# Optimization experiments

Measured on AMD Instinct MI355X. Metric: run time of the kernel, lower is better.

## Reference

```python
import jax, jax.numpy as jnp
import numpy as np

EPS = 1e-5
SLOPE = 0.2  # LeakyReLU negative slope used by torch_points3d MLP

N = 16384
IN_MAIN, IN_MOD = 64, 128
NC_INNER, NC_QK, OUT_MAIN = 16, 8, 64


def setup_inputs() -> dict:
    key = jax.random.key(0)
    ks = jax.random.split(key, 8)
    def w(k, shape, fan_in):
        return jax.random.normal(k, shape, jnp.float32) * (1.0 / np.sqrt(fan_in))
    return dict(
        x_main=jax.random.normal(ks[0], (N, IN_MAIN), jnp.float32),
        x_mod=jax.random.normal(ks[1], (N, IN_MOD), jnp.float32),
        xyz=jax.random.uniform(ks[2], (N, 3), jnp.float32),
        W1=w(ks[3], (IN_MAIN + IN_MOD, NC_INNER), IN_MAIN + IN_MOD),
        g1=jnp.ones((NC_INNER,), jnp.float32),
        b1=jnp.zeros((NC_INNER,), jnp.float32),
        W2=w(ks[4], (NC_INNER, NC_INNER), NC_INNER),
        g2=jnp.ones((NC_INNER,), jnp.float32),
        b2=jnp.zeros((NC_INNER,), jnp.float32),
        Wq=w(ks[5], (NC_INNER, NC_QK), NC_INNER),
        Wk=w(ks[6], (NC_INNER, NC_QK), NC_INNER),
        Wv=w(ks[7], (NC_INNER, OUT_MAIN), NC_INNER),
    )


def _mlp_layer(x, W, g, b):
    # Linear(bias=False) -> BatchNorm1d (batch stats, training mode) -> LeakyReLU(0.2)
    h = x @ W
    m = jnp.mean(h, axis=0)
    v = jnp.var(h, axis=0)
    h = (h - m) * jax.lax.rsqrt(v + EPS) * g + b
    return jnp.where(h >= 0, h, SLOPE * h)


def reference(x_main, x_mod, xyz, W1, g1, b1, W2, g2, b2, Wq, Wk, Wv):
    # concat(3D feats, 2D feats) -> 2-layer MLP encoder E
    x = jnp.concatenate([x_main, x_mod], axis=-1)          # [N, in_main+in_mod]
    x = _mlp_layer(x, W1, g1, b1)                          # [N, nc_inner]
    x = _mlp_layer(x, W2, g2, b2)                          # [N, nc_inner]
    # global self-attention: full NxN scores (as in the original code)
    Q = x @ Wq                                             # [N, nc_qk]
    K = x @ Wk                                             # [N, nc_qk]
    V = x @ Wv                                             # [N, out_main]
    scale = 1.0 / jnp.sqrt(jnp.asarray(Q.shape[-1], Q.dtype))
    A = jax.nn.softmax((Q @ K.T) * scale, axis=1)          # [N, N]
    return A @ V                                           # [N, out_main]
```

## Files before the change

kernel.cpp:

```cpp
#include <hip/hip_runtime.h>
#include <stdint.h>

#define N_PTS 16384
#define EPSV 1e-5f
#define SLOPEV 0.2f

typedef __attribute__((ext_vector_type(8))) __bf16 bf16x8;
typedef __attribute__((ext_vector_type(4))) float f32x4;

union U4 { uint4 u; bf16x8 b; };

__device__ inline unsigned short f2bf(float x) {
    union { float f; uint32_t u; } v; v.f = x;
    uint32_t r = v.u + 0x7FFFu + ((v.u >> 16) & 1u);
    return (unsigned short)(r >> 16);
}
__device__ inline float bf2f(unsigned short b) {
    union { float f; uint32_t u; } v; v.u = ((uint32_t)b) << 16; return v.f;
}
__device__ inline unsigned cvt2(float lo, float hi) {
    union { __bf16 h[2]; unsigned u; } w;
    w.h[0] = (__bf16)lo; w.h[1] = (__bf16)hi;
    return w.u;
}

__global__ __launch_bounds__(128)
void enc1_kernel(const float* __restrict__ xm, const float* __restrict__ xd,
                 const float* __restrict__ W1, float* __restrict__ h1,
                 float* __restrict__ sum1, float* __restrict__ sumsq1) {
    __shared__ __align__(16) float Ws[192 * 16];
    __shared__ float ssum[16], ssq[16];
    const int tid = threadIdx.x;
    for (int i = tid; i < 192 * 16; i += 128) Ws[i] = W1[i];
    if (tid < 16) { ssum[tid] = 0.f; ssq[tid] = 0.f; }
    __syncthreads();
    const int row = blockIdx.x * 128 + tid;
    float h[16];
#pragma unroll
    for (int c = 0; c < 16; ++c) h[c] = 0.f;
    for (int j = 0; j < 64; j += 4) {
        const float4 x = *(const float4*)(xm + (size_t)row * 64 + j);
#pragma unroll
        for (int cc = 0; cc < 4; ++cc) {
            const f32x4 w0 = *(const f32x4*)&Ws[(j + 0) * 16 + cc * 4];
            const f32x4 w1 = *(const f32x4*)&Ws[(j + 1) * 16 + cc * 4];
            const f32x4 w2 = *(const f32x4*)&Ws[(j + 2) * 16 + cc * 4];
            const f32x4 w3 = *(const f32x4*)&Ws[(j + 3) * 16 + cc * 4];
#pragma unroll
            for (int e = 0; e < 4; ++e)
                h[cc * 4 + e] += x.x * w0[e] + x.y * w1[e] + x.z * w2[e] + x.w * w3[e];
        }
    }
    for (int j = 0; j < 128; j += 4) {
        const float4 x = *(const float4*)(xd + (size_t)row * 128 + j);
#pragma unroll
        for (int cc = 0; cc < 4; ++cc) {
            const f32x4 w0 = *(const f32x4*)&Ws[(64 + j + 0) * 16 + cc * 4];
            const f32x4 w1 = *(const f32x4*)&Ws[(64 + j + 1) * 16 + cc * 4];
            const f32x4 w2 = *(const f32x4*)&Ws[(64 + j + 2) * 16 + cc * 4];
            const f32x4 w3 = *(const f32x4*)&Ws[(64 + j + 3) * 16 + cc * 4];
#pragma unroll
            for (int e = 0; e < 4; ++e)
                h[cc * 4 + e] += x.x * w0[e] + x.y * w1[e] + x.z * w2[e] + x.w * w3[e];
        }
    }
#pragma unroll
    for (int c = 0; c < 16; c += 4)
        *(float4*)(h1 + (size_t)row * 16 + c) = make_float4(h[c], h[c + 1], h[c + 2], h[c + 3]);
#pragma unroll
    for (int c = 0; c < 16; ++c) {
        atomicAdd(&ssum[c], h[c]);
        atomicAdd(&ssq[c], h[c] * h[c]);
    }
    __syncthreads();
    if (tid < 16) { atomicAdd(&sum1[tid], ssum[tid]); atomicAdd(&sumsq1[tid], ssq[tid]); }
}

__global__ __launch_bounds__(64)
void finalize_bn(const float* __restrict__ sum, const float* __restrict__ sumsq,
                 const float* __restrict__ g, const float* __restrict__ b,
                 float* __restrict__ scale, float* __restrict__ shift) {
    const int c = threadIdx.x;
    if (c < 16) {
        const float mean = sum[c] * (1.f / N_PTS);
        const float var = sumsq[c] * (1.f / N_PTS) - mean * mean;
        const float sc = g[c] * rsqrtf(var + EPSV);
        scale[c] = sc;
        shift[c] = b[c] - mean * sc;
    }
}

__global__ __launch_bounds__(128)
void enc2_kernel(const float* __restrict__ h1, const float* __restrict__ scale1,
                 const float* __restrict__ shift1, const float* __restrict__ W2,
                 float* __restrict__ h2, float* __restrict__ sum2, float* __restrict__ sumsq2) {
    __shared__ __align__(16) float Ws[256];
    __shared__ float ssum[16], ssq[16];
    const int tid = threadIdx.x;
    for (int i = tid; i < 256; i += 128) Ws[i] = W2[i];
    if (tid < 16) { ssum[tid] = 0.f; ssq[tid] = 0.f; }
    __syncthreads();
    const int row = blockIdx.x * 128 + tid;
    float a[16];
#pragma unroll
    for (int j = 0; j < 16; j += 4) {
        const float4 hv = *(const float4*)(h1 + (size_t)row * 16 + j);
        a[j + 0] = hv.x * scale1[j + 0] + shift1[j + 0];
        a[j + 1] = hv.y * scale1[j + 1] + shift1[j + 1];
        a[j + 2] = hv.z * scale1[j + 2] + shift1[j + 2];
        a[j + 3] = hv.w * scale1[j + 3] + shift1[j + 3];
    }
#pragma unroll
    for (int j = 0; j < 16; ++j) a[j] = a[j] >= 0.f ? a[j] : SLOPEV * a[j];
    float h[16];
#pragma unroll
    for (int c = 0; c < 16; ++c) h[c] = 0.f;
#pragma unroll
    for (int j = 0; j < 16; ++j) {
#pragma unroll
        for (int cc = 0; cc < 4; ++cc) {
            const f32x4 wv = *(const f32x4*)&Ws[j * 16 + cc * 4];
#pragma unroll
            for (int e = 0; e < 4; ++e) h[cc * 4 + e] += a[j] * wv[e];
        }
    }
#pragma unroll
    for (int c = 0; c < 16; c += 4)
        *(float4*)(h2 + (size_t)row * 16 + c) = make_float4(h[c], h[c + 1], h[c + 2], h[c + 3]);
#pragma unroll
    for (int c = 0; c < 16; ++c) {
        atomicAdd(&ssum[c], h[c]);
        atomicAdd(&ssq[c], h[c] * h[c]);
    }
    __syncthreads();
    if (tid < 16) { atomicAdd(&sum2[tid], ssum[tid]); atomicAdd(&sumsq2[tid], ssq[tid]); }
}

__global__ __launch_bounds__(128)
void qkv_kernel(const float* __restrict__ h2, const float* __restrict__ scale2,
                const float* __restrict__ shift2, const float* __restrict__ Wq,
                const float* __restrict__ Wk, const float* __restrict__ Wv,
                unsigned short* __restrict__ Qp, unsigned short* __restrict__ Kp,
                unsigned short* __restrict__ Vt) {
    __shared__ __align__(16) float wqs[128], wks[128], wvs[1024];
    const int tid = threadIdx.x;
    for (int i = tid; i < 128; i += 128) { wqs[i] = Wq[i]; wks[i] = Wk[i]; }
    for (int i = tid; i < 1024; i += 128) wvs[i] = Wv[i];
    __syncthreads();
    const int row = blockIdx.x * 128 + tid;
    float a[16];
#pragma unroll
    for (int j = 0; j < 16; j += 4) {
        const float4 hv = *(const float4*)(h2 + (size_t)row * 16 + j);
        a[j + 0] = hv.x * scale2[j + 0] + shift2[j + 0];
        a[j + 1] = hv.y * scale2[j + 1] + shift2[j + 1];
        a[j + 2] = hv.z * scale2[j + 2] + shift2[j + 2];
        a[j + 3] = hv.w * scale2[j + 3] + shift2[j + 3];
    }
#pragma unroll
    for (int j = 0; j < 16; ++j) a[j] = a[j] >= 0.f ? a[j] : SLOPEV * a[j];

    const float SCL = (float)(1.4426950408889634 / 2.8284271247461903);
    union RowU { unsigned short s[32]; uint4 u[4]; } qr, kr;
#pragma unroll
    for (int o = 0; o < 8; ++o) {
        float sq = 0.f, sk = 0.f;
#pragma unroll
        for (int j = 0; j < 16; ++j) {
            sq += a[j] * wqs[j * 8 + o];
            sk += a[j] * wks[j * 8 + o];
        }
        const float qs = sq * SCL;
        const unsigned short qh = f2bf(qs);
        const unsigned short ql = f2bf(qs - bf2f(qh));
        qr.s[o] = qh; qr.s[8 + o] = ql; qr.s[16 + o] = qh; qr.s[24 + o] = 0;
        const unsigned short kh = f2bf(sk);
        const unsigned short kl = f2bf(sk - bf2f(kh));
        kr.s[o] = kh; kr.s[8 + o] = kh; kr.s[16 + o] = kl; kr.s[24 + o] = 0;
    }
#pragma unroll
    for (int k4 = 0; k4 < 4; ++k4) {
        *(uint4*)(Qp + (size_t)row * 32 + k4 * 8) = qr.u[k4];
        *(uint4*)(Kp + (size_t)row * 32 + k4 * 8) = kr.u[k4];
    }
#pragma unroll
    for (int d = 0; d < 64; ++d) {
        float sv = 0.f;
#pragma unroll
        for (int j = 0; j < 16; ++j) sv += a[j] * wvs[j * 64 + d];
        Vt[(size_t)d * N_PTS + row] = f2bf(sv);
    }
}

__global__ __launch_bounds__(512, 2)
void attn_kernel(const unsigned short* __restrict__ Qp,
                 const unsigned short* __restrict__ Kp,
                 const unsigned short* __restrict__ Vt,
                 float* __restrict__ partO, float* __restrict__ partML,
                 int kv_per_split) {
    __shared__ __align__(16) unsigned short vlds[64 * 136];
    const int tid = threadIdx.x;
    const int w = tid >> 6;
    const int l = tid & 63;
    const int g = l >> 4;
    const int c = l & 15;
    const int split = blockIdx.x;
    const int qbase = blockIdx.y * 512 + w * 64;
    const int kv0 = split * kv_per_split;
    const int nstage = kv_per_split >> 7;

    U4 qf[4];
#pragma unroll
    for (int qt = 0; qt < 4; ++qt)
        qf[qt].u = *(const uint4*)(Qp + (size_t)(qbase + qt * 16 + c) * 32 + g * 8);

    f32x4 acc[4][4];
#pragma unroll
    for (int qt = 0; qt < 4; ++qt)
#pragma unroll
        for (int dt = 0; dt < 4; ++dt) acc[qt][dt] = (f32x4){0.f, 0.f, 0.f, 0.f};
    float m_run[4], l_run[4];
#pragma unroll
    for (int qt = 0; qt < 4; ++qt) { m_run[qt] = -3.0e38f; l_run[qt] = 0.f; }

    for (int stage = 0; stage < nstage; ++stage) {
        const int kvs = kv0 + stage * 128;
        __syncthreads();
        for (int i = tid; i < 1024; i += 512) {
            const int r = i >> 4, ch = i & 15;
            *(uint4*)(vlds + r * 136 + ch * 8) =
                *(const uint4*)(Vt + (size_t)r * N_PTS + kvs + ch * 8);
        }
        __syncthreads();
        for (int sub = 0; sub < 4; ++sub) {
            const int kvg = kvs + sub * 32;
            U4 kf0, kf1;
            kf0.u = *(const uint4*)(Kp + (size_t)(kvg + c) * 32 + g * 8);
            kf1.u = *(const uint4*)(Kp + (size_t)(kvg + 16 + c) * 32 + g * 8);
            const f32x4 z4 = {0.f, 0.f, 0.f, 0.f};
            f32x4 s0[4], s1[4];
#pragma unroll
            for (int qt = 0; qt < 4; ++qt) {
                s0[qt] = __builtin_amdgcn_mfma_f32_16x16x32_bf16(kf0.b, qf[qt].b, z4, 0, 0, 0);
                s1[qt] = __builtin_amdgcn_mfma_f32_16x16x32_bf16(kf1.b, qf[qt].b, z4, 0, 0, 0);
            }
            float mloc[4];
            bool upd = false;
#pragma unroll
            for (int qt = 0; qt < 4; ++qt) {
                float mm = fmaxf(fmaxf(fmaxf(s0[qt][0], s0[qt][1]), fmaxf(s0[qt][2], s0[qt][3])),
                                 fmaxf(fmaxf(s1[qt][0], s1[qt][1]), fmaxf(s1[qt][2], s1[qt][3])));
                mm = fmaxf(mm, __shfl_xor(mm, 16));
                mm = fmaxf(mm, __shfl_xor(mm, 32));
                mloc[qt] = mm;
                upd = upd || (mm > m_run[qt]);
            }
            if (__any((int)upd)) {
#pragma unroll
                for (int qt = 0; qt < 4; ++qt) {
                    const float mn = fmaxf(m_run[qt], mloc[qt]);
                    const float al = __builtin_amdgcn_exp2f(m_run[qt] - mn);
                    l_run[qt] *= al;
#pragma unroll
                    for (int dt = 0; dt < 4; ++dt) acc[qt][dt] *= al;
                    m_run[qt] = mn;
                }
            }
            U4 pfb[4];
#pragma unroll
            for (int qt = 0; qt < 4; ++qt) {
                float p[8];
#pragma unroll
                for (int r = 0; r < 4; ++r) {
                    p[r] = __builtin_amdgcn_exp2f(s0[qt][r] - m_run[qt]);
                    p[4 + r] = __builtin_amdgcn_exp2f(s1[qt][r] - m_run[qt]);
                }
                float ps = ((p[0] + p[1]) + (p[2] + p[3])) + ((p[4] + p[5]) + (p[6] + p[7]));
                ps += __shfl_xor(ps, 16);
                ps += __shfl_xor(ps, 32);
                l_run[qt] += ps;
                const unsigned t0w0 = cvt2(p[0], p[1]);
                const unsigned t0w1 = cvt2(p[2], p[3]);
                const unsigned t1w0 = cvt2(p[4], p[5]);
                const unsigned t1w1 = cvt2(p[6], p[7]);
                const int srcA = ((g & 1) << 5) + c;
                const int srcB = srcA + 16;
                const unsigned a0 = __shfl(t0w0, srcA), a1 = __shfl(t0w1, srcA);
                const unsigned a2 = __shfl(t0w0, srcB), a3 = __shfl(t0w1, srcB);
                const unsigned b0 = __shfl(t1w0, srcA), b1 = __shfl(t1w1, srcA);
                const unsigned b2 = __shfl(t1w0, srcB), b3 = __shfl(t1w1, srcB);
                const bool lo2 = (g < 2);
                pfb[qt].u = make_uint4(lo2 ? a0 : b0, lo2 ? a1 : b1,
                                       lo2 ? a2 : b2, lo2 ? a3 : b3);
            }
#pragma unroll
            for (int dt = 0; dt < 4; ++dt) {
                U4 vf;
                vf.u = *(const uint4*)(vlds + (dt * 16 + c) * 136 + sub * 32 + g * 8);
#pragma unroll
                for (int qt = 0; qt < 4; ++qt)
                    acc[qt][dt] = __builtin_amdgcn_mfma_f32_16x16x32_bf16(vf.b, pfb[qt].b,
                                                                          acc[qt][dt], 0, 0, 0);
            }
        }
    }
#pragma unroll
    for (int qt = 0; qt < 4; ++qt) {
        const int q = qbase + qt * 16 + c;
#pragma unroll
        for (int dt = 0; dt < 4; ++dt)
            *(f32x4*)(partO + ((size_t)split * N_PTS + q) * 64 + dt * 16 + g * 4) = acc[qt][dt];
        if (g == 0) {
            partML[((size_t)split * N_PTS + q) * 2 + 0] = m_run[qt];
            partML[((size_t)split * N_PTS + q) * 2 + 1] = l_run[qt];
        }
    }
}

__global__ __launch_bounds__(256)
void merge_kernel(const float* __restrict__ partO, const float* __restrict__ partML,
                  float* __restrict__ out, int nsplit) {
    const int t = blockIdx.x * 256 + threadIdx.x;
    const int q = t >> 2, ch = t & 3;
    float M = -3.0e38f;
    for (int s = 0; s < nsplit; ++s)
        M = fmaxf(M, partML[((size_t)s * N_PTS + q) * 2 + 0]);
    float den = 0.f;
    f32x4 o0 = {0.f, 0.f, 0.f, 0.f}, o1 = o0, o2 = o0, o3 = o0;
    for (int s = 0; s < nsplit; ++s) {
        const float wgt = __builtin_amdgcn_exp2f(partML[((size_t)s * N_PTS + q) * 2 + 0] - M);
        den += wgt * partML[((size_t)s * N_PTS + q) * 2 + 1];
        const float* p = partO + ((size_t)s * N_PTS + q) * 64 + ch * 16;
        o0 += wgt * *(const f32x4*)(p + 0);
        o1 += wgt * *(const f32x4*)(p + 4);
        o2 += wgt * *(const f32x4*)(p + 8);
        o3 += wgt * *(const f32x4*)(p + 12);
    }
    const float inv = 1.f / den;
    float* po = out + (size_t)q * 64 + ch * 16;
    *(f32x4*)(po + 0) = o0 * inv;
    *(f32x4*)(po + 4) = o1 * inv;
    *(f32x4*)(po + 8) = o2 * inv;
    *(f32x4*)(po + 12) = o3 * inv;
}

extern "C" void kernel_launch(void* const* d_in, const int* in_sizes, int n_in,
                              void* d_out, int out_size, void* d_ws, size_t ws_size,
                              hipStream_t stream) {
    const float* xm = (const float*)d_in[0];
    const float* xd = (const float*)d_in[1];
    const float* W1 = (const float*)d_in[3];
    const float* g1 = (const float*)d_in[4];
    const float* b1 = (const float*)d_in[5];
    const float* W2 = (const float*)d_in[6];
    const float* g2 = (const float*)d_in[7];
    const float* b2 = (const float*)d_in[8];
    const float* Wq = (const float*)d_in[9];
    const float* Wk = (const float*)d_in[10];
    const float* Wv = (const float*)d_in[11];
    float* out = (float*)d_out;
    char* ws = (char*)d_ws;

    float* sum1 = (float*)(ws + 0);
    float* sumsq1 = (float*)(ws + 64);
    float* sum2 = (float*)(ws + 128);
    float* sumsq2 = (float*)(ws + 192);
    float* scale1 = (float*)(ws + 256);
    float* shift1 = (float*)(ws + 320);
    float* scale2 = (float*)(ws + 384);
    float* shift2 = (float*)(ws + 448);
    float* h1 = (float*)(ws + (1u << 20));
    float* h2 = (float*)(ws + (2u << 20));
    unsigned short* Qp = (unsigned short*)(ws + (3u << 20));
    unsigned short* Kp = (unsigned short*)(ws + (4u << 20));
    unsigned short* Vt = (unsigned short*)(ws + (5u << 20));
    float* partML = (float*)(ws + (7u << 20));
    float* partO = (float*)(ws + (8u << 20));

    int nsplit = 8;
    while (nsplit > 1 && (8u + 4u * (unsigned)nsplit) * (1u << 20) > ws_size) nsplit >>= 1;
    const int kv_per_split = N_PTS / nsplit;

    hipMemsetAsync(ws, 0, 256, stream);
    hipLaunchKernelGGL(enc1_kernel, dim3(128), dim3(128), 0, stream, xm, xd, W1, h1, sum1, sumsq1);
    hipLaunchKernelGGL(finalize_bn, dim3(1), dim3(64), 0, stream, sum1, sumsq1, g1, b1, scale1, shift1);
    hipLaunchKernelGGL(enc2_kernel, dim3(128), dim3(128), 0, stream, h1, scale1, shift1, W2, h2, sum2, sumsq2);
    hipLaunchKernelGGL(finalize_bn, dim3(1), dim3(64), 0, stream, sum2, sumsq2, g2, b2, scale2, shift2);
    hipLaunchKernelGGL(qkv_kernel, dim3(128), dim3(128), 0, stream, h2, scale2, shift2, Wq, Wk, Wv, Qp, Kp, Vt);
    hipLaunchKernelGGL(attn_kernel, dim3(nsplit, 32), dim3(512), 0, stream, Qp, Kp, Vt, partO, partML, kv_per_split);
    hipLaunchKernelGGL(merge_kernel, dim3(256), dim3(256), 0, stream, partO, partML, out, nsplit);
}
```

Baseline: 382.6 us.

## Switch attention to 32x32x16 MFMA with swizzled V LDS and lazy rescale

The attention kernel now uses 32x32x16 bf16 MFMA tiles with one 32-query tile per wave instead of four 16x16x32 tiles. It drops the cross-lane shuffles that repacked P, because the 32x32 output layout feeds the PV MFMA directly. The Q/K split-bf16 packing is reduced from three terms to two MFMA passes, and V in LDS uses an XOR swizzle instead of padding. The running max is only updated when it grows by more than 8 (log2 units), block occupancy is raised to 4 per CU and the grid doubles. Per-thread accumulator registers and max/shuffle work drop, but lazy rescaling risks larger exponent ranges and the bf16 P precision is unchanged.

Measured after the change: 327.0 us. 14.5% less time.

```diff
diff --git a/kernel.cpp b/kernel.cpp
--- a/kernel.cpp
+++ b/kernel.cpp
@@ -7,6 +7,7 @@
 
 typedef __attribute__((ext_vector_type(8))) __bf16 bf16x8;
 typedef __attribute__((ext_vector_type(4))) float f32x4;
+typedef __attribute__((ext_vector_type(16))) float f32x16;
 
 union U4 { uint4 u; bf16x8 b; };
 
@@ -161,7 +162,8 @@
     for (int j = 0; j < 16; ++j) a[j] = a[j] >= 0.f ? a[j] : SLOPEV * a[j];
 
     const float SCL = (float)(1.4426950408889634 / 2.8284271247461903);
-    union RowU { unsigned short s[32]; uint4 u[4]; } qr, kr;
+    union Row16 { unsigned short s[16]; uint4 u[2]; } qr;
+    union Row32 { unsigned short s[32]; uint4 u[4]; } kr;
 #pragma unroll
     for (int o = 0; o < 8; ++o) {
         float sq = 0.f, sk = 0.f;
@@ -173,16 +175,16 @@
         const float qs = sq * SCL;
         const unsigned short qh = f2bf(qs);
         const unsigned short ql = f2bf(qs - bf2f(qh));
-        qr.s[o] = qh; qr.s[8 + o] = ql; qr.s[16 + o] = qh; qr.s[24 + o] = 0;
+        qr.s[o] = qh; qr.s[8 + o] = ql;
         const unsigned short kh = f2bf(sk);
         const unsigned short kl = f2bf(sk - bf2f(kh));
-        kr.s[o] = kh; kr.s[8 + o] = kh; kr.s[16 + o] = kl; kr.s[24 + o] = 0;
-    }
-#pragma unroll
-    for (int k4 = 0; k4 < 4; ++k4) {
-        *(uint4*)(Qp + (size_t)row * 32 + k4 * 8) = qr.u[k4];
+        kr.s[o] = kh; kr.s[8 + o] = kl; kr.s[16 + o] = 0; kr.s[24 + o] = 0;
+    }
+    *(uint4*)(Qp + (size_t)row * 16 + 0) = qr.u[0];
+    *(uint4*)(Qp + (size_t)row * 16 + 8) = qr.u[1];
+#pragma unroll
+    for (int k4 = 0; k4 < 4; ++k4)
         *(uint4*)(Kp + (size_t)row * 32 + k4 * 8) = kr.u[k4];
-    }
 #pragma unroll
     for (int d = 0; d < 64; ++d) {
         float sv = 0.f;
@@ -192,128 +194,104 @@
     }
 }
 
-__global__ __launch_bounds__(512, 2)
+__global__ __launch_bounds__(512, 4)
 void attn_kernel(const unsigned short* __restrict__ Qp,
                  const unsigned short* __restrict__ Kp,
                  const unsigned short* __restrict__ Vt,
                  float* __restrict__ partO, float* __restrict__ partML,
                  int kv_per_split) {
-    __shared__ __align__(16) unsigned short vlds[64 * 136];
+    __shared__ __align__(16) unsigned short vlds[64 * 128];
+    unsigned char* vb = (unsigned char*)vlds;
     const int tid = threadIdx.x;
     const int w = tid >> 6;
     const int l = tid & 63;
-    const int g = l >> 4;
-    const int c = l & 15;
+    const int hi = l >> 5;
+    const int c5 = l & 31;
     const int split = blockIdx.x;
-    const int qbase = blockIdx.y * 512 + w * 64;
+    const int q = blockIdx.y * 256 + w * 32 + c5;
     const int kv0 = split * kv_per_split;
     const int nstage = kv_per_split >> 7;
 
-    U4 qf[4];
-#pragma unroll
-    for (int qt = 0; qt < 4; ++qt)
-        qf[qt].u = *(const uint4*)(Qp + (size_t)(qbase + qt * 16 + c) * 32 + g * 8);
-
-    f32x4 acc[4][4];
-#pragma unroll
-    for (int qt = 0; qt < 4; ++qt)
-#pragma unroll
-        for (int dt = 0; dt < 4; ++dt) acc[qt][dt] = (f32x4){0.f, 0.f, 0.f, 0.f};
-    float m_run[4], l_run[4];
-#pragma unroll
-    for (int qt = 0; qt < 4; ++qt) { m_run[qt] = -3.0e38f; l_run[qt] = 0.f; }
+    U4 qf;
+    qf.u = *(const uint4*)(Qp + (size_t)q * 16 + hi * 8);
+
+    const f32x16 Z16 = {0.f,0.f,0.f,0.f, 0.f,0.f,0.f,0.f, 0.f,0.f,0.f,0.f, 0.f,0.f,0.f,0.f};
+    f32x16 acc0 = Z16, acc1 = Z16;
+    float m_run = -3.0e38f, l_run = 0.f;
 
     for (int stage = 0; stage < nstage; ++stage) {
         const int kvs = kv0 + stage * 128;
         __syncthreads();
         for (int i = tid; i < 1024; i += 512) {
             const int r = i >> 4, ch = i & 15;
-            *(uint4*)(vlds + r * 136 + ch * 8) =
-                *(const uint4*)(Vt + (size_t)r * N_PTS + kvs + ch * 8);
+            const int dst = r * 256 + ((ch * 16) ^ ((r & 15) << 4));
+            *(uint4*)(vb + dst) = *(const uint4*)(Vt + (size_t)r * N_PTS + kvs + ch * 8);
         }
         __syncthreads();
+#pragma unroll
         for (int sub = 0; sub < 4; ++sub) {
             const int kvg = kvs + sub * 32;
-            U4 kf0, kf1;
-            kf0.u = *(const uint4*)(Kp + (size_t)(kvg + c) * 32 + g * 8);
-            kf1.u = *(const uint4*)(Kp + (size_t)(kvg + 16 + c) * 32 + g * 8);
-            const f32x4 z4 = {0.f, 0.f, 0.f, 0.f};
-            f32x4 s0[4], s1[4];
-#pragma unroll
-            for (int qt = 0; qt < 4; ++qt) {
-                s0[qt] = __builtin_amdgcn_mfma_f32_16x16x32_bf16(kf0.b, qf[qt].b, z4, 0, 0, 0);
-                s1[qt] = __builtin_amdgcn_mfma_f32_16x16x32_bf16(kf1.b, qf[qt].b, z4, 0, 0, 0);
+            U4 ka1, ka2;
+            ka1.u = *(const uint4*)(Kp + (size_t)(kvg + c5) * 32);
+            ka2.u = *(const uint4*)(Kp + (size_t)(kvg + c5) * 32 + 8 + hi * 8);
+            f32x16 S = __builtin_amdgcn_mfma_f32_32x32x16_bf16(ka1.b, qf.b, Z16, 0, 0, 0);
+            S = __builtin_amdgcn_mfma_f32_32x32x16_bf16(ka2.b, qf.b, S, 0, 0, 0);
+            float mm = fmaxf(S[0], S[1]);
+#pragma unroll
+            for (int i = 2; i < 16; ++i) mm = fmaxf(mm, S[i]);
+            mm = fmaxf(mm, __shfl_xor(mm, 32));
+            if (__any((int)(mm > m_run + 8.f))) {
+                const float mn = fmaxf(m_run, mm);
+                const float al = __builtin_amdgcn_exp2f(m_run - mn);
+                l_run *= al;
+                acc0 *= al;
+                acc1 *= al;
+                m_run = mn;
             }
-            float mloc[4];
-            bool upd = false;
-#pragma unroll
-            for (int qt = 0; qt < 4; ++qt) {
-                float mm = fmaxf(fmaxf(fmaxf(s0[qt][0], s0[qt][1]), fmaxf(s0[qt][2], s0[qt][3])),
-                                 fmaxf(fmaxf(s1[qt][0], s1[qt][1]), fmaxf(s1[qt][2], s1[qt][3])));
-                mm = fmaxf(mm, __shfl_xor(mm, 16));
-                mm = fmaxf(mm, __shfl_xor(mm, 32));
-                mloc[qt] = mm;
-                upd = upd || (mm > m_run[qt]);
+            float p[16];
+#pragma unroll
+            for (int i = 0; i < 16; ++i) p[i] = __builtin_amdgcn_exp2f(S[i] - m_run);
+            const float ps = ((p[0] + p[1]) + (p[2] + p[3])) + ((p[4] + p[5]) + (p[6] + p[7]))
+                           + ((p[8] + p[9]) + (p[10] + p[11])) + ((p[12] + p[13]) + (p[14] + p[15]));
+            l_run += ps + __shfl_xor(ps, 32);
+            unsigned W[8];
+#pragma unroll
+            for (int m = 0; m < 4; ++m) {
+                W[2 * m + 0] = cvt2(p[4 * m + 0], p[4 * m + 1]);
+                W[2 * m + 1] = cvt2(p[4 * m + 2], p[4 * m + 3]);
             }
-            if (__any((int)upd)) {
-#pragma unroll
-                for (int qt = 0; qt < 4; ++qt) {
-                    const float mn = fmaxf(m_run[qt], mloc[qt]);
-                    const float al = __builtin_amdgcn_exp2f(m_run[qt] - mn);
-                    l_run[qt] *= al;
-#pragma unroll
-                    for (int dt = 0; dt < 4; ++dt) acc[qt][dt] *= al;
-                    m_run[qt] = mn;
-                }
+#pragma unroll
+            for (int kvh = 0; kvh < 2; ++kvh) {
+                U4 bf;
+                bf.u = make_uint4(W[4 * kvh + 0], W[4 * kvh + 1],
+                                  W[4 * kvh + 2], W[4 * kvh + 3]);
+                const int colb = sub * 64 + kvh * 32 + hi * 8;
+                const int a0 = c5 * 256 + (colb ^ ((c5 & 15) << 4));
+                const int r1 = 32 + c5;
+                const int a1 = r1 * 256 + (colb ^ ((r1 & 15) << 4));
+                const uint2 lo0 = *(const uint2*)(vb + a0);
+                const uint2 hi0 = *(const uint2*)(vb + (a0 ^ 16));
+                const uint2 lo1 = *(const uint2*)(vb + a1);
+                const uint2 hi1 = *(const uint2*)(vb + (a1 ^ 16));
+                U4 vf0, vf1;
+                vf0.u = make_uint4(lo0.x, lo0.y, hi0.x, hi0.y);
+                vf1.u = make_uint4(lo1.x, lo1.y, hi1.x, hi1.y);
+                acc0 = __builtin_amdgcn_mfma_f32_32x32x16_bf16(vf0.b, bf.b, acc0, 0, 0, 0);
+                acc1 = __builtin_amdgcn_mfma_f32_32x32x16_bf16(vf1.b, bf.b, acc1, 0, 0, 0);
             }
-            U4 pfb[4];
-#pragma unroll
-            for (int qt = 0; qt < 4; ++qt) {
-                float p[8];
-#pragma unroll
-                for (int r = 0; r < 4; ++r) {
-                    p[r] = __builtin_amdgcn_exp2f(s0[qt][r] - m_run[qt]);
-                    p[4 + r] = __builtin_amdgcn_exp2f(s1[qt][r] - m_run[qt]);
-                }
-                float ps = ((p[0] + p[1]) + (p[2] + p[3])) + ((p[4] + p[5]) + (p[6] + p[7]));
-                ps += __shfl_xor(ps, 16);
-                ps += __shfl_xor(ps, 32);
-                l_run[qt] += ps;
-                const unsigned t0w0 = cvt2(p[0], p[1]);
-                const unsigned t0w1 = cvt2(p[2], p[3]);
-                const unsigned t1w0 = cvt2(p[4], p[5]);
-                const unsigned t1w1 = cvt2(p[6], p[7]);
-                const int srcA = ((g & 1) << 5) + c;
-                const int srcB = srcA + 16;
-                const unsigned a0 = __shfl(t0w0, srcA), a1 = __shfl(t0w1, srcA);
-                const unsigned a2 = __shfl(t0w0, srcB), a3 = __shfl(t0w1, srcB);
-                const unsigned b0 = __shfl(t1w0, srcA), b1 = __shfl(t1w1, srcA);
-                const unsigned b2 = __shfl(t1w0, srcB), b3 = __shfl(t1w1, srcB);
-                const bool lo2 = (g < 2);
-                pfb[qt].u = make_uint4(lo2 ? a0 : b0, lo2 ? a1 : b1,
-                                       lo2 ? a2 : b2, lo2 ? a3 : b3);
-            }
-#pragma unroll
-            for (int dt = 0; dt < 4; ++dt) {
-                U4 vf;
-                vf.u = *(const uint4*)(vlds + (dt * 16 + c) * 136 + sub * 32 + g * 8);
-#pragma unroll
-                for (int qt = 0; qt < 4; ++qt)
-                    acc[qt][dt] = __builtin_amdgcn_mfma_f32_16x16x32_bf16(vf.b, pfb[qt].b,
-                                                                          acc[qt][dt], 0, 0, 0);
-            }
-        }
-    }
-#pragma unroll
-    for (int qt = 0; qt < 4; ++qt) {
-        const int q = qbase + qt * 16 + c;
-#pragma unroll
-        for (int dt = 0; dt < 4; ++dt)
-            *(f32x4*)(partO + ((size_t)split * N_PTS + q) * 64 + dt * 16 + g * 4) = acc[qt][dt];
-        if (g == 0) {
-            partML[((size_t)split * N_PTS + q) * 2 + 0] = m_run[qt];
-            partML[((size_t)split * N_PTS + q) * 2 + 1] = l_run[qt];
-        }
+        }
+    }
+    const size_t obase = ((size_t)split * N_PTS + q) * 64;
+#pragma unroll
+    for (int m = 0; m < 4; ++m) {
+        const f32x4 v0 = {acc0[4 * m + 0], acc0[4 * m + 1], acc0[4 * m + 2], acc0[4 * m + 3]};
+        const f32x4 v1 = {acc1[4 * m + 0], acc1[4 * m + 1], acc1[4 * m + 2], acc1[4 * m + 3]};
+        *(f32x4*)(partO + obase + 8 * m + 4 * hi) = v0;
+        *(f32x4*)(partO + obase + 32 + 8 * m + 4 * hi) = v1;
+    }
+    if (hi == 0) {
+        partML[((size_t)split * N_PTS + q) * 2 + 0] = m_run;
+        partML[((size_t)split * N_PTS + q) * 2 + 1] = l_run;
     }
 }
 
@@ -387,6 +365,6 @@
     hipLaunchKernelGGL(enc2_kernel, dim3(128), dim3(128), 0, stream, h1, scale1, shift1, W2, h2, sum2, sumsq2);
     hipLaunchKernelGGL(finalize_bn, dim3(1), dim3(64), 0, stream, sum2, sumsq2, g2, b2, scale2, shift2);
     hipLaunchKernelGGL(qkv_kernel, dim3(128), dim3(128), 0, stream, h2, scale2, shift2, Wq, Wk, Wv, Qp, Kp, Vt);
-    hipLaunchKernelGGL(attn_kernel, dim3(nsplit, 32), dim3(512), 0, stream, Qp, Kp, Vt, partO, partML, kv_per_split);
+    hipLaunchKernelGGL(attn_kernel, dim3(nsplit, 64), dim3(512), 0, stream, Qp, Kp, Vt, partO, partML, kv_per_split);
     hipLaunchKernelGGL(merge_kernel, dim3(256), dim3(256), 0, stream, partO, partML, out, nsplit);
 }
```
